# Optimization experiments

Measured on AMD Instinct MI355X. Metric: run time of the kernel, lower is better.

Reference implementation:

```python
import jax, jax.numpy as jnp
import numpy as np
import math

HIDDEN = 256
N_HEADS = 4
MAX_NB = 64  # max neighbors per sample (segment length cap)
B = 4096
N_TOTAL = 131072


def setup_inputs() -> dict:
    key = jax.random.key(0)
    ks = jax.random.split(key, 12)
    enc_hidden = jax.random.normal(ks[0], (B, HIDDEN), dtype=jnp.float32)
    social_ht = jax.random.normal(ks[1], (N_TOTAL, HIDDEN), dtype=jnp.float32)
    # contiguous ragged segments: start in [0, N_TOTAL-MAX_NB], len in [1, MAX_NB]
    starts = jnp.sort(jax.random.randint(ks[2], (B,), 0, N_TOTAL - MAX_NB, dtype=jnp.int32))
    lens = jax.random.randint(ks[3], (B,), 1, MAX_NB + 1, dtype=jnp.int32)
    ends = starts + lens
    s = 1.0 / math.sqrt(HIDDEN)
    def lin(k):
        kw, kb = jax.random.split(k)
        W = jax.random.uniform(kw, (HIDDEN, HIDDEN), jnp.float32, -s, s)
        b = jax.random.uniform(kb, (HIDDEN,), jnp.float32, -s, s)
        return W, b
    Wq, bq = lin(ks[4])
    Wk, bk = lin(ks[5])
    Wv, bv = lin(ks[6])
    Wf, bf = lin(ks[7])
    return {
        "enc_hidden": enc_hidden, "social_ht": social_ht,
        "Wq": Wq, "bq": bq, "Wk": Wk, "bk": bk, "Wv": Wv, "bv": bv,
        "Wf": Wf, "bf": bf,
        "neighbors_idx_start": starts, "neighbors_idx_end": ends,
    }


def reference(enc_hidden, social_ht, Wq, bq, Wk, bk, Wv, bv, Wf, bf,
              neighbors_idx_start, neighbors_idx_end):
    b, h = enc_hidden.shape
    dh = h // N_HEADS
    # query: Linear+ReLU then scale by sqrt(feat_dim) (as in source)
    q = jax.nn.relu(enc_hidden @ Wq.T + bq) / jnp.sqrt(jnp.float32(h))  # [B,H]
    # gather padded contiguous neighbor segments
    idx = neighbors_idx_start[:, None] + jnp.arange(MAX_NB, dtype=neighbors_idx_start.dtype)  # [B,M]
    valid = idx < neighbors_idx_end[:, None]  # [B,M]
    ht = social_ht[jnp.clip(idx, 0, social_ht.shape[0] - 1)]  # [B,M,H]
    k = jax.nn.relu(ht @ Wk.T + bk)  # [B,M,H]
    v = jax.nn.relu(ht @ Wv.T + bv)  # [B,M,H]
    qh = q.reshape(b, N_HEADS, dh)            # [B,h,d]
    kh = k.reshape(b, MAX_NB, N_HEADS, dh)    # [B,M,h,d]
    vh = v.reshape(b, MAX_NB, N_HEADS, dh)
    scores = jnp.einsum('bhd,bmhd->bhm', qh, kh)
    scores = jnp.where(valid[:, None, :], scores, jnp.float32(-1e30))
    attn = jax.nn.softmax(scores, axis=-1)    # [B,h,M]
    out = jnp.einsum('bhm,bmhd->bhd', attn, vh).reshape(b, h)
    return out @ Wf.T + bf
```

## Files before the change

### kernel.cpp

```cpp
#include <hip/hip_runtime.h>
#include <hip/hip_bf16.h>

typedef __attribute__((ext_vector_type(8))) short bf16x8;
typedef __attribute__((ext_vector_type(4))) float f32x4;
typedef __attribute__((ext_vector_type(4))) unsigned short us4;

__device__ __forceinline__ unsigned short f2bf(float f) {
    unsigned int u = __builtin_bit_cast(unsigned int, f);
    unsigned int r = (u + 0x7FFFu + ((u >> 16) & 1u)) >> 16;
    return (unsigned short)r;
}
__device__ __forceinline__ float bf2f(unsigned short h) {
    unsigned int u = ((unsigned int)h) << 16;
    return __builtin_bit_cast(float, u);
}

__device__ __forceinline__ void gload_lds16(const void* g, void* l) {
    __builtin_amdgcn_global_load_lds(
        (const __attribute__((address_space(1))) unsigned int*)g,
        (__attribute__((address_space(3))) unsigned int*)l, 16, 0, 0);
}

__global__ __launch_bounds__(512, 4) void kv_gemm_rb(
    const float* __restrict__ A,
    const float* __restrict__ Wk, const float* __restrict__ bk,
    const float* __restrict__ Wv, const float* __restrict__ bv,
    unsigned short* __restrict__ KV2)
{
    __shared__ unsigned short Abuf[2][32 * 256];

    const int tid = threadIdx.x;
    const int wave = tid >> 6, lane = tid & 63;

    const int g = (blockIdx.x & 7) * 128 + (blockIdx.x >> 3);
    const int colhalf = g & 1;
    const size_t mb = (size_t)(g >> 1) * 256;
    const int colbase = colhalf * 256 + wave * 32;

    bf16x8 bfrag[2][8];
    float biasr[2][4];
    int inner0[2];
    #pragma unroll
    for (int ni = 0; ni < 2; ++ni) {
        int jcol = colbase + ni * 16 + (lane & 15);
        const float* Wr = (jcol < 256) ? (Wk + (size_t)jcol * 256)
                                       : (Wv + (size_t)(jcol - 256) * 256);
        #pragma unroll
        for (int ks = 0; ks < 8; ++ks) {
            int k0 = ks * 32 + ((lane >> 4) << 3);
            float4 x = *(const float4*)(Wr + k0);
            float4 y = *(const float4*)(Wr + k0 + 4);
            bf16x8 f;
            f[0] = (short)f2bf(x.x); f[1] = (short)f2bf(x.y);
            f[2] = (short)f2bf(x.z); f[3] = (short)f2bf(x.w);
            f[4] = (short)f2bf(y.x); f[5] = (short)f2bf(y.y);
            f[6] = (short)f2bf(y.z); f[7] = (short)f2bf(y.w);
            bfrag[ni][ks] = f;
        }
        int j0 = colbase + ni * 16 + ((lane >> 4) << 2);
        const float* bsrc = (j0 < 256) ? (bk + j0) : (bv + j0 - 256);
        float4 bb = *(const float4*)bsrc;
        biasr[ni][0] = bb.x; biasr[ni][1] = bb.y; biasr[ni][2] = bb.z; biasr[ni][3] = bb.w;
        if (j0 < 256) inner0[ni] = (j0 >> 6) * 128 + (j0 & 63);
        else { int t2 = j0 - 256; inner0[ni] = (t2 >> 6) * 128 + 64 + (t2 & 63); }
    }

    const int srow = tid >> 4, sseg = tid & 15;
    const int sbyte0 = srow * 512 + sseg * 32;
    const int ssw = (srow & 7) << 4;

    {
        const float* src = A + (mb + srow) * 256 + sseg * 16;
        float4 a0 = *(const float4*)(src + 0);
        float4 a1 = *(const float4*)(src + 4);
        float4 a2 = *(const float4*)(src + 8);
        float4 a3 = *(const float4*)(src + 12);
        us4 h0, h1, h2, h3;
        h0.x=f2bf(a0.x); h0.y=f2bf(a0.y); h0.z=f2bf(a0.z); h0.w=f2bf(a0.w);
        h1.x=f2bf(a1.x); h1.y=f2bf(a1.y); h1.z=f2bf(a1.z); h1.w=f2bf(a1.w);
        h2.x=f2bf(a2.x); h2.y=f2bf(a2.y); h2.z=f2bf(a2.z); h2.w=f2bf(a2.w);
        h3.x=f2bf(a3.x); h3.y=f2bf(a3.y); h3.z=f2bf(a3.z); h3.w=f2bf(a3.w);
        char* dst = (char*)Abuf[0];
        *(us4*)(dst + ((sbyte0 +  0) ^ ssw)) = h0;
        *(us4*)(dst + ((sbyte0 +  8) ^ ssw)) = h1;
        *(us4*)(dst + ((sbyte0 + 16) ^ ssw)) = h2;
        *(us4*)(dst + ((sbyte0 + 24) ^ ssw)) = h3;
    }
    __syncthreads();

    for (int t = 0; t < 8; ++t) {
        const bool pf = (t + 1) < 8;
        float4 a0, a1, a2, a3;
        if (pf) {
            const float* src = A + (mb + (t + 1) * 32 + srow) * 256 + sseg * 16;
            a0 = *(const float4*)(src + 0);
            a1 = *(const float4*)(src + 4);
            a2 = *(const float4*)(src + 8);
            a3 = *(const float4*)(src + 12);
        }

        f32x4 acc[2][2] = {};
        const char* Ab = (const char*)Abuf[t & 1];
        #pragma unroll
        for (int ks = 0; ks < 8; ++ks) {
            bf16x8 af[2];
            #pragma unroll
            for (int mi = 0; mi < 2; ++mi) {
                int row = mi * 16 + (lane & 15);
                int byte = row * 512 + ks * 64 + ((lane >> 4) << 4);
                af[mi] = *(const bf16x8*)(Ab + (byte ^ ((row & 7) << 4)));
            }
            #pragma unroll
            for (int ni = 0; ni < 2; ++ni)
                #pragma unroll
                for (int mi = 0; mi < 2; ++mi)
                    acc[mi][ni] = __builtin_amdgcn_mfma_f32_16x16x32_bf16(
                        bfrag[ni][ks], af[mi], acc[mi][ni], 0, 0, 0);
        }

        #pragma unroll
        for (int ni = 0; ni < 2; ++ni) {
            #pragma unroll
            for (int mi = 0; mi < 2; ++mi) {
                size_t m = mb + (size_t)t * 32 + mi * 16 + (lane & 15);
                us4 h;
                #pragma unroll
                for (int r = 0; r < 4; ++r)
                    h[r] = f2bf(fmaxf(acc[mi][ni][r] + biasr[ni][r], 0.f));
                *(us4*)(KV2 + m * 512 + inner0[ni]) = h;
            }
        }

        if (pf) {
            us4 h0, h1, h2, h3;
            h0.x=f2bf(a0.x); h0.y=f2bf(a0.y); h0.z=f2bf(a0.z); h0.w=f2bf(a0.w);
            h1.x=f2bf(a1.x); h1.y=f2bf(a1.y); h1.z=f2bf(a1.z); h1.w=f2bf(a1.w);
            h2.x=f2bf(a2.x); h2.y=f2bf(a2.y); h2.z=f2bf(a2.z); h2.w=f2bf(a2.w);
            h3.x=f2bf(a3.x); h3.y=f2bf(a3.y); h3.z=f2bf(a3.z); h3.w=f2bf(a3.w);
            char* dst = (char*)Abuf[(t + 1) & 1];
            *(us4*)(dst + ((sbyte0 +  0) ^ ssw)) = h0;
            *(us4*)(dst + ((sbyte0 +  8) ^ ssw)) = h1;
            *(us4*)(dst + ((sbyte0 + 16) ^ ssw)) = h2;
            *(us4*)(dst + ((sbyte0 + 24) ^ ssw)) = h3;
        }
        __syncthreads();
    }
}

template<int RELU>
__global__ __launch_bounds__(256) void gemm_proj(
    const float* __restrict__ A, const float* __restrict__ W,
    const float* __restrict__ bias, float* __restrict__ out, float scale)
{
    __shared__ unsigned short As[64 * 256];
    __shared__ unsigned short Bs[64 * 256];
    char* AsB = (char*)As;
    char* BsB = (char*)Bs;

    const int tid = threadIdx.x;
    const int wave = tid >> 6, lane = tid & 63;
    const int m0 = blockIdx.x * 64;
    const int jbase = blockIdx.y * 64;

    #pragma unroll
    for (int i = 0; i < 4; ++i) {
        int f = tid + i * 256;
        int row = f >> 4, seg = f & 15;
        int byte0 = row * 512 + seg * 32;
        int sw = (row & 7) << 4;
        {
            const float* pa = A + (size_t)(m0 + row) * 256 + seg * 16;
            float4 a0 = *(const float4*)(pa + 0);
            float4 a1 = *(const float4*)(pa + 4);
            float4 a2 = *(const float4*)(pa + 8);
            float4 a3 = *(const float4*)(pa + 12);
            us4 h0, h1, h2, h3;
            h0.x=f2bf(a0.x); h0.y=f2bf(a0.y); h0.z=f2bf(a0.z); h0.w=f2bf(a0.w);
            h1.x=f2bf(a1.x); h1.y=f2bf(a1.y); h1.z=f2bf(a1.z); h1.w=f2bf(a1.w);
            h2.x=f2bf(a2.x); h2.y=f2bf(a2.y); h2.z=f2bf(a2.z); h2.w=f2bf(a2.w);
            h3.x=f2bf(a3.x); h3.y=f2bf(a3.y); h3.z=f2bf(a3.z); h3.w=f2bf(a3.w);
            *(us4*)(AsB + ((byte0 +  0) ^ sw)) = h0;
            *(us4*)(AsB + ((byte0 +  8) ^ sw)) = h1;
            *(us4*)(AsB + ((byte0 + 16) ^ sw)) = h2;
            *(us4*)(AsB + ((byte0 + 24) ^ sw)) = h3;
        }
        {
            const float* pw = W + (size_t)(jbase + row) * 256 + seg * 16;
            float4 a0 = *(const float4*)(pw + 0);
            float4 a1 = *(const float4*)(pw + 4);
            float4 a2 = *(const float4*)(pw + 8);
            float4 a3 = *(const float4*)(pw + 12);
            us4 h0, h1, h2, h3;
            h0.x=f2bf(a0.x); h0.y=f2bf(a0.y); h0.z=f2bf(a0.z); h0.w=f2bf(a0.w);
            h1.x=f2bf(a1.x); h1.y=f2bf(a1.y); h1.z=f2bf(a1.z); h1.w=f2bf(a1.w);
            h2.x=f2bf(a2.x); h2.y=f2bf(a2.y); h2.z=f2bf(a2.z); h2.w=f2bf(a2.w);
            h3.x=f2bf(a3.x); h3.y=f2bf(a3.y); h3.z=f2bf(a3.z); h3.w=f2bf(a3.w);
            *(us4*)(BsB + ((byte0 +  0) ^ sw)) = h0;
            *(us4*)(BsB + ((byte0 +  8) ^ sw)) = h1;
            *(us4*)(BsB + ((byte0 + 16) ^ sw)) = h2;
            *(us4*)(BsB + ((byte0 + 24) ^ sw)) = h3;
        }
    }
    __syncthreads();

    f32x4 acc[4] = {};
    #pragma unroll
    for (int ks = 0; ks < 8; ++ks) {
        int arow = wave * 16 + (lane & 15);
        int abyte = arow * 512 + ks * 64 + ((lane >> 4) << 4);
        bf16x8 af = *(const bf16x8*)(AsB + (abyte ^ ((arow & 7) << 4)));
        #pragma unroll
        for (int ni = 0; ni < 4; ++ni) {
            int brow = ni * 16 + (lane & 15);
            int bbyte = brow * 512 + ks * 64 + ((lane >> 4) << 4);
            bf16x8 bfr = *(const bf16x8*)(BsB + (bbyte ^ ((brow & 7) << 4)));
            acc[ni] = __builtin_amdgcn_mfma_f32_16x16x32_bf16(bfr, af, acc[ni], 0, 0, 0);
        }
    }

    int m = m0 + wave * 16 + (lane & 15);
    #pragma unroll
    for (int ni = 0; ni < 4; ++ni) {
        int j0 = jbase + ni * 16 + ((lane >> 4) << 2);
        float4 bb = *(const float4*)(bias + j0);
        float4 o;
        o.x = acc[ni][0] + bb.x; o.y = acc[ni][1] + bb.y;
        o.z = acc[ni][2] + bb.z; o.w = acc[ni][3] + bb.w;
        if (RELU) {
            o.x = fmaxf(o.x, 0.f); o.y = fmaxf(o.y, 0.f);
            o.z = fmaxf(o.z, 0.f); o.w = fmaxf(o.w, 0.f);
        }
        o.x *= scale; o.y *= scale; o.z *= scale; o.w *= scale;
        *(float4*)(out + (size_t)m * 256 + j0) = o;
    }
}

__global__ __launch_bounds__(64) void attn_kernel(
    const float* __restrict__ Q, const unsigned short* __restrict__ KV2,
    const int* __restrict__ starts, const int* __restrict__ ends,
    float* __restrict__ out)
{
    __shared__ unsigned short kvs[64 * 128];
    __shared__ float qs[64];
    __shared__ float aw[64];

    const int bid = blockIdx.x;
    const int idx = ((bid & 7) << 11) | (bid >> 3);
    const int b = idx >> 2, h = idx & 3;
    const int ln = threadIdx.x;
    const int start = starts[b];
    const int len = ends[b] - start;

    {
        const int r4 = ln >> 4, c = ln & 15;
        #pragma unroll
        for (int i = 0; i < 16; ++i) {
            if (i * 4 < len) {
                int rr = i * 4 + r4;
                const char* src = (const char*)(KV2 + (size_t)(start + rr) * 512 + h * 128)
                                  + ((c * 16) ^ ((rr & 7) << 4));
                gload_lds16(src, (char*)kvs + i * 1024 + ln * 16);
            }
        }
    }
    qs[ln] = Q[(size_t)b * 256 + h * 64 + ln];
    __syncthreads();

    float2 qreg[32];
    #pragma unroll
    for (int j = 0; j < 32; ++j)
        qreg[j] = *(const float2*)(qs + 2 * j);

    float sx = 0.f, sy = 0.f;
    {
        const char* krow = (const char*)kvs + ln * 256;
        const int sw = (ln & 7) << 4;
        #pragma unroll
        for (int j8 = 0; j8 < 8; ++j8) {
            bf16x8 kf = *(const bf16x8*)(krow + ((j8 * 16) ^ sw));
            #pragma unroll
            for (int p = 0; p < 4; ++p) {
                float2 q2 = qreg[j8 * 4 + p];
                sx = fmaf(q2.x, bf2f((unsigned short)kf[2 * p]), sx);
                sy = fmaf(q2.y, bf2f((unsigned short)kf[2 * p + 1]), sy);
            }
        }
    }
    float s = (ln < len) ? (sx + sy) : -3.0e38f;
    float mx = s;
    #pragma unroll
    for (int off = 32; off; off >>= 1) mx = fmaxf(mx, __shfl_xor(mx, off));
    float e = (ln < len) ? __expf(s - mx) : 0.f;
    float sum = e;
    #pragma unroll
    for (int off = 32; off; off >>= 1) sum += __shfl_xor(sum, off);
    aw[ln] = e / sum;
    __syncthreads();

    const int half = ln >> 5, dl = ln & 31;
    int nm = len - half * 32; nm = nm < 0 ? 0 : (nm > 32 ? 32 : nm);
    float a0 = 0.f, a1 = 0.f;
    const char* vb = (const char*)kvs + half * 32 * 256;
    const int voff = 128 + dl * 4;
    for (int mm = 0; mm < nm; ++mm) {
        unsigned int vv = *(const unsigned int*)(vb + mm * 256 + (voff ^ ((mm & 7) << 4)));
        float awm = aw[half * 32 + mm];
        a0 = fmaf(awm, __builtin_bit_cast(float, vv << 16), a0);
        a1 = fmaf(awm, __builtin_bit_cast(float, vv & 0xFFFF0000u), a1);
    }
    a0 += __shfl_xor(a0, 32);
    a1 += __shfl_xor(a1, 32);
    if (ln < 32) {
        float2 o; o.x = a0; o.y = a1;
        *(float2*)(out + (size_t)b * 256 + h * 64 + 2 * dl) = o;
    }
}

extern "C" void kernel_launch(void* const* d_in, const int* in_sizes, int n_in,
                              void* d_out, int out_size, void* d_ws, size_t ws_size,
                              hipStream_t stream) {
    const float* enc    = (const float*)d_in[0];
    const float* social = (const float*)d_in[1];
    const float* Wq = (const float*)d_in[2];
    const float* bq = (const float*)d_in[3];
    const float* Wk = (const float*)d_in[4];
    const float* bk = (const float*)d_in[5];
    const float* Wv = (const float*)d_in[6];
    const float* bv = (const float*)d_in[7];
    const float* Wf = (const float*)d_in[8];
    const float* bf = (const float*)d_in[9];
    const int* st = (const int*)d_in[10];
    const int* en = (const int*)d_in[11];
    (void)in_sizes; (void)n_in; (void)out_size; (void)ws_size;

    char* ws = (char*)d_ws;
    unsigned short* KV2 = (unsigned short*)ws;
    float* Qb    = (float*)(ws + 134217728);
    float* attnb = (float*)(ws + 134217728 + 4194304);
    float* outf  = (float*)d_out;

    kv_gemm_rb<<<dim3(1024), dim3(512), 0, stream>>>(social, Wk, bk, Wv, bv, KV2);
    gemm_proj<1><<<dim3(64, 4), dim3(256), 0, stream>>>(enc, Wq, bq, Qb, 0.0625f);
    attn_kernel<<<dim3(16384), dim3(64), 0, stream>>>(Qb, KV2, st, en, attnb);
    gemm_proj<0><<<dim3(64, 4), dim3(256), 0, stream>>>(attnb, Wf, bf, outf, 1.0f);
}
```

Measured before the change: 355.7 us.

## Restructure KV GEMM to register-streamed A and per-sample multi-head attention blocks

The KV projection kernel drops the LDS double buffer and loads A fragments straight from global into registers. Each block now covers all 512 output columns for its 256 rows, so A is read once instead of twice, at the cost of more registers and no prefetch overlap. The KV layout becomes plain K[256] then V[256] per row. The attention kernel now runs one 256-thread block per sample with the four heads as waves, sharing a single K load into LDS, while V is read directly from global. The Q-projection GEMM switches to scalar loads.

```diff
diff --git a/kernel.cpp b/kernel.cpp
--- a/kernel.cpp
+++ b/kernel.cpp
@@ -21,129 +21,83 @@
         (__attribute__((address_space(3))) unsigned int*)l, 16, 0, 0);
 }
 
-__global__ __launch_bounds__(512, 4) void kv_gemm_rb(
+__device__ __forceinline__ bf16x8 pack8(float4 x, float4 y) {
+    bf16x8 f;
+    f[0] = (short)f2bf(x.x); f[1] = (short)f2bf(x.y);
+    f[2] = (short)f2bf(x.z); f[3] = (short)f2bf(x.w);
+    f[4] = (short)f2bf(y.x); f[5] = (short)f2bf(y.y);
+    f[6] = (short)f2bf(y.z); f[7] = (short)f2bf(y.w);
+    return f;
+}
+
+__global__ __launch_bounds__(512, 2) void kv_stream(
     const float* __restrict__ A,
     const float* __restrict__ Wk, const float* __restrict__ bk,
     const float* __restrict__ Wv, const float* __restrict__ bv,
-    unsigned short* __restrict__ KV2)
+    unsigned short* __restrict__ KV)
 {
-    __shared__ unsigned short Abuf[2][32 * 256];
-
     const int tid = threadIdx.x;
-    const int wave = tid >> 6, lane = tid & 63;
-
-    const int g = (blockIdx.x & 7) * 128 + (blockIdx.x >> 3);
-    const int colhalf = g & 1;
-    const size_t mb = (size_t)(g >> 1) * 256;
-    const int colbase = colhalf * 256 + wave * 32;
-
-    bf16x8 bfrag[2][8];
-    float biasr[2][4];
-    int inner0[2];
-    #pragma unroll
-    for (int ni = 0; ni < 2; ++ni) {
-        int jcol = colbase + ni * 16 + (lane & 15);
-        const float* Wr = (jcol < 256) ? (Wk + (size_t)jcol * 256)
-                                       : (Wv + (size_t)(jcol - 256) * 256);
+    const int w = tid >> 6, l = tid & 63;
+    const int lg = l >> 4, lr = l & 15;
+    const size_t mb = (size_t)blockIdx.x * 256;
+
+    const int cb = w * 64;
+    const float* Wbase = (w < 4) ? Wk : Wv;
+    const float* bbase = (w < 4) ? bk : bv;
+    const int cw = (w & 3) * 64;
+
+    bf16x8 bfrag[4][8];
+    float biasv[4][4];
+    #pragma unroll
+    for (int ni = 0; ni < 4; ++ni) {
+        const float* Wr = Wbase + (size_t)(cw + ni * 16 + lr) * 256;
         #pragma unroll
         for (int ks = 0; ks < 8; ++ks) {
-            int k0 = ks * 32 + ((lane >> 4) << 3);
-            float4 x = *(const float4*)(Wr + k0);
-            float4 y = *(const float4*)(Wr + k0 + 4);
-            bf16x8 f;
-            f[0] = (short)f2bf(x.x); f[1] = (short)f2bf(x.y);
-            f[2] = (short)f2bf(x.z); f[3] = (short)f2bf(x.w);
-            f[4] = (short)f2bf(y.x); f[5] = (short)f2bf(y.y);
-            f[6] = (short)f2bf(y.z); f[7] = (short)f2bf(y.w);
-            bfrag[ni][ks] = f;
-        }
-        int j0 = colbase + ni * 16 + ((lane >> 4) << 2);
-        const float* bsrc = (j0 < 256) ? (bk + j0) : (bv + j0 - 256);
-        float4 bb = *(const float4*)bsrc;
-        biasr[ni][0] = bb.x; biasr[ni][1] = bb.y; biasr[ni][2] = bb.z; biasr[ni][3] = bb.w;
-        if (j0 < 256) inner0[ni] = (j0 >> 6) * 128 + (j0 & 63);
-        else { int t2 = j0 - 256; inner0[ni] = (t2 >> 6) * 128 + 64 + (t2 & 63); }
-    }
-
-    const int srow = tid >> 4, sseg = tid & 15;
-    const int sbyte0 = srow * 512 + sseg * 32;
-    const int ssw = (srow & 7) << 4;
-
-    {
-        const float* src = A + (mb + srow) * 256 + sseg * 16;
-        float4 a0 = *(const float4*)(src + 0);
-        float4 a1 = *(const float4*)(src + 4);
-        float4 a2 = *(const float4*)(src + 8);
-        float4 a3 = *(const float4*)(src + 12);
-        us4 h0, h1, h2, h3;
-        h0.x=f2bf(a0.x); h0.y=f2bf(a0.y); h0.z=f2bf(a0.z); h0.w=f2bf(a0.w);
-        h1.x=f2bf(a1.x); h1.y=f2bf(a1.y); h1.z=f2bf(a1.z); h1.w=f2bf(a1.w);
-        h2.x=f2bf(a2.x); h2.y=f2bf(a2.y); h2.z=f2bf(a2.z); h2.w=f2bf(a2.w);
-        h3.x=f2bf(a3.x); h3.y=f2bf(a3.y); h3.z=f2bf(a3.z); h3.w=f2bf(a3.w);
-        char* dst = (char*)Abuf[0];
-        *(us4*)(dst + ((sbyte0 +  0) ^ ssw)) = h0;
-        *(us4*)(dst + ((sbyte0 +  8) ^ ssw)) = h1;
-        *(us4*)(dst + ((sbyte0 + 16) ^ ssw)) = h2;
-        *(us4*)(dst + ((sbyte0 + 24) ^ ssw)) = h3;
-    }
-    __syncthreads();
+            const float* p = Wr + ks * 32 + lg * 8;
+            bfrag[ni][ks] = pack8(*(const float4*)p, *(const float4*)(p + 4));
+        }
+        float4 bb = *(const float4*)(bbase + cw + ni * 16 + lg * 4);
+        biasv[ni][0] = bb.x; biasv[ni][1] = bb.y;
+        biasv[ni][2] = bb.z; biasv[ni][3] = bb.w;
+    }
 
     for (int t = 0; t < 8; ++t) {
-        const bool pf = (t + 1) < 8;
-        float4 a0, a1, a2, a3;
-        if (pf) {
-            const float* src = A + (mb + (t + 1) * 32 + srow) * 256 + sseg * 16;
-            a0 = *(const float4*)(src + 0);
-            a1 = *(const float4*)(src + 4);
-            a2 = *(const float4*)(src + 8);
-            a3 = *(const float4*)(src + 12);
-        }
-
-        f32x4 acc[2][2] = {};
-        const char* Ab = (const char*)Abuf[t & 1];
-        #pragma unroll
-        for (int ks = 0; ks < 8; ++ks) {
-            bf16x8 af[2];
-            #pragma unroll
-            for (int mi = 0; mi < 2; ++mi) {
-                int row = mi * 16 + (lane & 15);
-                int byte = row * 512 + ks * 64 + ((lane >> 4) << 4);
-                af[mi] = *(const bf16x8*)(Ab + (byte ^ ((row & 7) << 4)));
+        const size_t r0 = mb + (size_t)t * 32;
+
+        bf16x8 af[2][8];
+        #pragma unroll
+        for (int mi = 0; mi < 2; ++mi) {
+            const float* Ar = A + (r0 + mi * 16 + lr) * 256;
+            #pragma unroll
+            for (int ks = 0; ks < 8; ++ks) {
+                const float* p = Ar + ks * 32 + lg * 8;
+                af[mi][ks] = pack8(*(const float4*)p, *(const float4*)(p + 4));
             }
-            #pragma unroll
-            for (int ni = 0; ni < 2; ++ni)
+        }
+
+        f32x4 acc[4][2] = {};
+        #pragma unroll
+        for (int ks = 0; ks < 8; ++ks)
+            #pragma unroll
+            for (int ni = 0; ni < 4; ++ni)
                 #pragma unroll
                 for (int mi = 0; mi < 2; ++mi)
-                    acc[mi][ni] = __builtin_amdgcn_mfma_f32_16x16x32_bf16(
-                        bfrag[ni][ks], af[mi], acc[mi][ni], 0, 0, 0);
-        }
-
-        #pragma unroll
-        for (int ni = 0; ni < 2; ++ni) {
+                    acc[ni][mi] = __builtin_amdgcn_mfma_f32_16x16x32_bf16(
+                        bfrag[ni][ks], af[mi][ks], acc[ni][mi], 0, 0, 0);
+
+        #pragma unroll
+        for (int ni = 0; ni < 4; ++ni) {
+            const int j0 = cb + ni * 16 + lg * 4;
             #pragma unroll
             for (int mi = 0; mi < 2; ++mi) {
-                size_t m = mb + (size_t)t * 32 + mi * 16 + (lane & 15);
+                size_t m = r0 + mi * 16 + lr;
                 us4 h;
                 #pragma unroll
                 for (int r = 0; r < 4; ++r)
-                    h[r] = f2bf(fmaxf(acc[mi][ni][r] + biasr[ni][r], 0.f));
-                *(us4*)(KV2 + m * 512 + inner0[ni]) = h;
+                    h[r] = f2bf(fmaxf(acc[ni][mi][r] + biasv[ni][r], 0.f));
+                *(us4*)(KV + m * 512 + j0) = h;
             }
         }
-
-        if (pf) {
-            us4 h0, h1, h2, h3;
-            h0.x=f2bf(a0.x); h0.y=f2bf(a0.y); h0.z=f2bf(a0.z); h0.w=f2bf(a0.w);
-            h1.x=f2bf(a1.x); h1.y=f2bf(a1.y); h1.z=f2bf(a1.z); h1.w=f2bf(a1.w);
-            h2.x=f2bf(a2.x); h2.y=f2bf(a2.y); h2.z=f2bf(a2.z); h2.w=f2bf(a2.w);
-            h3.x=f2bf(a3.x); h3.y=f2bf(a3.y); h3.z=f2bf(a3.z); h3.w=f2bf(a3.w);
-            char* dst = (char*)Abuf[(t + 1) & 1];
-            *(us4*)(dst + ((sbyte0 +  0) ^ ssw)) = h0;
-            *(us4*)(dst + ((sbyte0 +  8) ^ ssw)) = h1;
-            *(us4*)(dst + ((sbyte0 + 16) ^ ssw)) = h2;
-            *(us4*)(dst + ((sbyte0 + 24) ^ ssw)) = h3;
-        }
-        __syncthreads();
     }
 }
 
@@ -170,15 +124,10 @@
         int sw = (row & 7) << 4;
         {
             const float* pa = A + (size_t)(m0 + row) * 256 + seg * 16;
-            float4 a0 = *(const float4*)(pa + 0);
-            float4 a1 = *(const float4*)(pa + 4);
-            float4 a2 = *(const float4*)(pa + 8);
-            float4 a3 = *(const float4*)(pa + 12);
-            us4 h0, h1, h2, h3;
-            h0.x=f2bf(a0.x); h0.y=f2bf(a0.y); h0.z=f2bf(a0.z); h0.w=f2bf(a0.w);
-            h1.x=f2bf(a1.x); h1.y=f2bf(a1.y); h1.z=f2bf(a1.z); h1.w=f2bf(a1.w);
-            h2.x=f2bf(a2.x); h2.y=f2bf(a2.y); h2.z=f2bf(a2.z); h2.w=f2bf(a2.w);
-            h3.x=f2bf(a3.x); h3.y=f2bf(a3.y); h3.z=f2bf(a3.z); h3.w=f2bf(a3.w);
+            us4 h0 = { f2bf(pa[0]), f2bf(pa[1]), f2bf(pa[2]), f2bf(pa[3]) };
+            us4 h1 = { f2bf(pa[4]), f2bf(pa[5]), f2bf(pa[6]), f2bf(pa[7]) };
+            us4 h2 = { f2bf(pa[8]), f2bf(pa[9]), f2bf(pa[10]), f2bf(pa[11]) };
+            us4 h3 = { f2bf(pa[12]), f2bf(pa[13]), f2bf(pa[14]), f2bf(pa[15]) };
             *(us4*)(AsB + ((byte0 +  0) ^ sw)) = h0;
             *(us4*)(AsB + ((byte0 +  8) ^ sw)) = h1;
             *(us4*)(AsB + ((byte0 + 16) ^ sw)) = h2;
@@ -186,15 +135,10 @@
         }
         {
             const float* pw = W + (size_t)(jbase + row) * 256 + seg * 16;
-            float4 a0 = *(const float4*)(pw + 0);
-            float4 a1 = *(const float4*)(pw + 4);
-            float4 a2 = *(const float4*)(pw + 8);
-            float4 a3 = *(const float4*)(pw + 12);
-            us4 h0, h1, h2, h3;
-            h0.x=f2bf(a0.x); h0.y=f2bf(a0.y); h0.z=f2bf(a0.z); h0.w=f2bf(a0.w);
-            h1.x=f2bf(a1.x); h1.y=f2bf(a1.y); h1.z=f2bf(a1.z); h1.w=f2bf(a1.w);
-            h2.x=f2bf(a2.x); h2.y=f2bf(a2.y); h2.z=f2bf(a2.z); h2.w=f2bf(a2.w);
-            h3.x=f2bf(a3.x); h3.y=f2bf(a3.y); h3.z=f2bf(a3.z); h3.w=f2bf(a3.w);
+            us4 h0 = { f2bf(pw[0]), f2bf(pw[1]), f2bf(pw[2]), f2bf(pw[3]) };
+            us4 h1 = { f2bf(pw[4]), f2bf(pw[5]), f2bf(pw[6]), f2bf(pw[7]) };
+            us4 h2 = { f2bf(pw[8]), f2bf(pw[9]), f2bf(pw[10]), f2bf(pw[11]) };
+            us4 h3 = { f2bf(pw[12]), f2bf(pw[13]), f2bf(pw[14]), f2bf(pw[15]) };
             *(us4*)(BsB + ((byte0 +  0) ^ sw)) = h0;
             *(us4*)(BsB + ((byte0 +  8) ^ sw)) = h1;
             *(us4*)(BsB + ((byte0 + 16) ^ sw)) = h2;
@@ -235,49 +179,44 @@
     }
 }
 
-__global__ __launch_bounds__(64) void attn_kernel(
-    const float* __restrict__ Q, const unsigned short* __restrict__ KV2,
+__global__ __launch_bounds__(256) void attn_kernel(
+    const float* __restrict__ Q, const unsigned short* __restrict__ KV,
     const int* __restrict__ starts, const int* __restrict__ ends,
     float* __restrict__ out)
 {
-    __shared__ unsigned short kvs[64 * 128];
-    __shared__ float qs[64];
-    __shared__ float aw[64];
+    __shared__ unsigned short kls[64 * 256];
+    __shared__ float qs[256];
+    __shared__ float aw[4][64];
 
     const int bid = blockIdx.x;
-    const int idx = ((bid & 7) << 11) | (bid >> 3);
-    const int b = idx >> 2, h = idx & 3;
-    const int ln = threadIdx.x;
+    const int b = ((bid & 7) << 9) | (bid >> 3);
+    const int t = threadIdx.x;
+    const int h = t >> 6, ln = t & 63;
     const int start = starts[b];
     const int len = ends[b] - start;
 
-    {
-        const int r4 = ln >> 4, c = ln & 15;
-        #pragma unroll
-        for (int i = 0; i < 16; ++i) {
-            if (i * 4 < len) {
-                int rr = i * 4 + r4;
-                const char* src = (const char*)(KV2 + (size_t)(start + rr) * 512 + h * 128)
-                                  + ((c * 16) ^ ((rr & 7) << 4));
-                gload_lds16(src, (char*)kvs + i * 1024 + ln * 16);
-            }
-        }
-    }
-    qs[ln] = Q[(size_t)b * 256 + h * 64 + ln];
+    const int nins = (len + 1) >> 1;
+    for (int i = h; i < nins; i += 4) {
+        int row = 2 * i + (ln >> 5);
+        const char* src = (const char*)(KV + (size_t)(start + row) * 512)
+                        + (((ln & 31) * 16) ^ ((row & 7) << 4));
+        gload_lds16(src, (char*)kls + i * 1024 + ln * 16);
+    }
+    qs[t] = Q[(size_t)b * 256 + t];
     __syncthreads();
 
     float2 qreg[32];
     #pragma unroll
     for (int j = 0; j < 32; ++j)
-        qreg[j] = *(const float2*)(qs + 2 * j);
+        qreg[j] = *(const float2*)(qs + h * 64 + 2 * j);
 
     float sx = 0.f, sy = 0.f;
     {
-        const char* krow = (const char*)kvs + ln * 256;
+        const char* krow = (const char*)kls + ln * 512;
         const int sw = (ln & 7) << 4;
         #pragma unroll
         for (int j8 = 0; j8 < 8; ++j8) {
-            bf16x8 kf = *(const bf16x8*)(krow + ((j8 * 16) ^ sw));
+            bf16x8 kf = *(const bf16x8*)(krow + ((h * 128 + j8 * 16) ^ sw));
             #pragma unroll
             for (int p = 0; p < 4; ++p) {
                 float2 q2 = qreg[j8 * 4 + p];
@@ -294,17 +233,15 @@
     float sum = e;
     #pragma unroll
     for (int off = 32; off; off >>= 1) sum += __shfl_xor(sum, off);
-    aw[ln] = e / sum;
-    __syncthreads();
+    aw[h][ln] = e / sum;
 
     const int half = ln >> 5, dl = ln & 31;
     int nm = len - half * 32; nm = nm < 0 ? 0 : (nm > 32 ? 32 : nm);
     float a0 = 0.f, a1 = 0.f;
-    const char* vb = (const char*)kvs + half * 32 * 256;
-    const int voff = 128 + dl * 4;
+    const unsigned short* vb = KV + (size_t)(start + half * 32) * 512 + 256 + h * 64 + 2 * dl;
     for (int mm = 0; mm < nm; ++mm) {
-        unsigned int vv = *(const unsigned int*)(vb + mm * 256 + (voff ^ ((mm & 7) << 4)));
-        float awm = aw[half * 32 + mm];
+        unsigned int vv = *(const unsigned int*)(vb + (size_t)mm * 512);
+        float awm = aw[h][half * 32 + mm];
         a0 = fmaf(awm, __builtin_bit_cast(float, vv << 16), a0);
         a1 = fmaf(awm, __builtin_bit_cast(float, vv & 0xFFFF0000u), a1);
     }
@@ -334,13 +271,13 @@
     (void)in_sizes; (void)n_in; (void)out_size; (void)ws_size;
 
     char* ws = (char*)d_ws;
-    unsigned short* KV2 = (unsigned short*)ws;
+    unsigned short* KV = (unsigned short*)ws;
     float* Qb    = (float*)(ws + 134217728);
     float* attnb = (float*)(ws + 134217728 + 4194304);
     float* outf  = (float*)d_out;
 
-    kv_gemm_rb<<<dim3(1024), dim3(512), 0, stream>>>(social, Wk, bk, Wv, bv, KV2);
+    kv_stream<<<dim3(512), dim3(512), 0, stream>>>(social, Wk, bk, Wv, bv, KV);
     gemm_proj<1><<<dim3(64, 4), dim3(256), 0, stream>>>(enc, Wq, bq, Qb, 0.0625f);
-    attn_kernel<<<dim3(16384), dim3(64), 0, stream>>>(Qb, KV2, st, en, attnb);
+    attn_kernel<<<dim3(4096), dim3(256), 0, stream>>>(Qb, KV, st, en, attnb);
     gemm_proj<0><<<dim3(64, 4), dim3(256), 0, stream>>>(attnb, Wf, bf, outf, 1.0f);
 }
```

New measurement: 423.9 us. 19.2% more time.
